# Optimization experiments

Measured on AMD Instinct MI355X. Metric: run time of the kernel, lower is better.

## Reference

```python
import jax, jax.numpy as jnp
import numpy as np

CONSTRAINT_WEIGHT = 0.5
FOCAL_GAMMA = 2.0
EPS = 1e-8

B, G, C = 65536, 9, 9
BLK = 3  # int(sqrt(G))


def setup_inputs() -> dict:
    key = jax.random.key(0)
    k1, k2, k3 = jax.random.split(key, 3)
    logits = jax.random.normal(k1, (B, G, G, C), dtype=jnp.float32)
    targets = jax.random.randint(k2, (B, G, G), 0, 10, dtype=jnp.int64)
    puzzles = jax.random.randint(k3, (B, G, G), 0, 10, dtype=jnp.int64)
    return {"logits": logits, "targets": targets, "puzzles": puzzles}


def _sudoku_loss(logits, targets, puzzles):
    b, g, _, c = logits.shape
    mask = (puzzles == 0).astype(logits.dtype)            # [B,G,G]
    tgt = jnp.clip(targets - 1, 0, c - 1)                 # [B,G,G]

    log_probs = jax.nn.log_softmax(logits, axis=-1)       # [B,G,G,C]
    probs = jnp.exp(log_probs)

    # --- focal CE over masked (empty) cells ---
    lp_t = jnp.take_along_axis(log_probs, tgt[..., None], axis=-1)[..., 0]  # [B,G,G]
    pt = jnp.exp(lp_t)
    ce = -lp_t
    focal = (1.0 - pt) ** FOCAL_GAMMA * ce
    msum = mask.sum()
    ce_loss = (focal * mask).sum() / (msum + EPS)

    # --- constraint loss ---
    masked_probs = probs * mask[..., None]                # [B,G,G,C]
    row_sums = masked_probs.sum(axis=2)                   # [B,G,C]
    row_loss = jnp.mean((row_sums - 1.0) ** 2)
    col_sums = masked_probs.sum(axis=1)                   # [B,G,C]
    col_loss = jnp.mean((col_sums - 1.0) ** 2)
    # boxes: [B, br, r, bc, c_in, C] -> sum over the 3x3 cells of each box
    box = masked_probs.reshape(b, BLK, BLK, BLK, BLK, c)
    box_sums = box.transpose(0, 1, 3, 2, 4, 5).reshape(b, BLK * BLK, BLK * BLK, c).sum(axis=2)
    box_loss = jnp.mean((box_sums - 1.0) ** 2)

    entropy = -(probs * log_probs).sum(axis=-1)           # [B,G,G]
    entropy_loss = 0.1 * ((entropy * mask).sum() / (msum + EPS))

    top2, _ = jax.lax.top_k(probs, 2)                     # [B,G,G,2]
    gap = top2[..., 0] - top2[..., 1]
    uniqueness_loss = 0.1 * jnp.mean(jax.nn.relu(1.0 - gap))

    constraint_loss = (row_loss + col_loss + box_loss + entropy_loss + uniqueness_loss) * 0.2
    return ce_loss + CONSTRAINT_WEIGHT * constraint_loss


def reference(logits, targets, puzzles):
    return _sudoku_loss(logits, targets, puzzles)
```

## Files before the change

### kernel.cpp

```cpp
#include <hip/hip_runtime.h>

#define THREADS 256
#define PB 3
#define NPAIR 5
#define COLW 84
#define MAXGRID 2048

typedef float f4 __attribute__((ext_vector_type(4)));
typedef f4 f4a4 __attribute__((aligned(4)));
typedef __fp16 h2 __attribute__((ext_vector_type(2)));
typedef unsigned int u32;
typedef u32 u32x4 __attribute__((ext_vector_type(4)));

static __device__ __forceinline__ u32 pkrtz(float a, float b) {
  h2 v = __builtin_amdgcn_cvt_pkrtz(a, b);
  return __builtin_bit_cast(u32, v);
}

__global__ __launch_bounds__(THREADS) void sudoku_main(
    const float* __restrict__ logits,
    const int*   __restrict__ targets,
    const int*   __restrict__ puzzles,
    float* __restrict__ partial,
    int B)
{
  __shared__ u32 probT[2][PB * NPAIR * COLW];
  __shared__ float sred[4][5];

  const int tid  = threadIdx.x;
  const int lp   = tid / 81;
  const int cell = tid % 81;
  const bool workerA = tid < 243;
  const int cpad = 28 * (cell / 27) + (cell % 27);
  const int B81  = B * 81;
  const int numGroups = (B + PB - 1) / PB;

  const int lane = tid & 63;
  const int wv   = tid >> 6;
  const int clp  = lane / NPAIR;
  const int cpr  = lane % NPAIR;

  float a_focal = 0.f, a_ent = 0.f, a_msk = 0.f, a_uniq = 0.f, a_sq = 0.f;

  bool vA = workerA && (blockIdx.x * 243 + tid < B81);
  f4 c0{}, c1{}; float c8 = 0.f; int ctg = 0, cpz = 0;
  if (vA) {
    const float* Lp = logits + (size_t)(blockIdx.x * 243 + tid) * 9;
    c0 = *(const f4a4*)Lp; c1 = *(const f4a4*)(Lp + 4); c8 = Lp[8];
    ctg = targets[blockIdx.x * 243 + tid]; cpz = puzzles[blockIdx.x * 243 + tid];
  }

  int it = 0;
  for (int g = blockIdx.x; g < numGroups; g += gridDim.x, ++it) {
    u32* PT = probT[it & 1];

    if (vA) {
      float l[9];
      l[0]=c0[0]; l[1]=c0[1]; l[2]=c0[2]; l[3]=c0[3];
      l[4]=c1[0]; l[5]=c1[1]; l[6]=c1[2]; l[7]=c1[3]; l[8]=c8;
      int tg = ctg - 1; tg = tg < 0 ? 0 : (tg > 8 ? 8 : tg);

      float t1 = l[0], t2 = -3.0e38f;
#pragma unroll
      for (int i = 1; i < 9; ++i) {
        float hi = fmaxf(t1, l[i]);
        float lo = fminf(t1, l[i]);
        t1 = hi; t2 = fmaxf(t2, lo);
      }
      float e[9], s = 0.f, lsum = 0.f, ltg = l[0];
#pragma unroll
      for (int i = 0; i < 9; ++i) {
        float x  = l[i] - t1;
        float ei = __expf(x);
        e[i] = ei; s += ei;
        lsum = fmaf(ei, x, lsum);
        if (i > 0) ltg = (tg == i) ? l[i] : ltg;
      }
      float inv_s = __builtin_amdgcn_rcpf(s);
      float logs  = __logf(s);
      float lpt   = (ltg - t1) - logs;
      float pt    = __expf(lpt);
      float om    = 1.f - pt;
      float focal = om * om * (-lpt);
      float ent   = logs - lsum * inv_s;
      float gap   = (1.f - __expf(t2 - t1)) * inv_s;
      float uq    = fmaxf(0.f, 1.f - gap);
      float mk    = (cpz == 0) ? 1.f : 0.f;
      a_focal += focal * mk;
      a_ent   += ent * mk;
      a_msk   += mk;
      a_uniq  += uq;
      float pm = inv_s * mk;

      const int wbase = lp * (NPAIR * COLW) + cpad;
      PT[wbase + 0*COLW] = pkrtz(e[0]*pm, e[1]*pm);
      PT[wbase + 1*COLW] = pkrtz(e[2]*pm, e[3]*pm);
      PT[wbase + 2*COLW] = pkrtz(e[4]*pm, e[5]*pm);
      PT[wbase + 3*COLW] = pkrtz(e[6]*pm, e[7]*pm);
      PT[wbase + 4*COLW] = pkrtz(e[8]*pm, 0.f);
    }

    const int gn = g + (int)gridDim.x;
    const bool vAn = workerA && (gn < numGroups) && (gn * 243 + tid < B81);
    f4 n0{}, n1{}; float n8 = 0.f; int ntg = 0, npz = 0;
    if (vAn) {
      const float* Lp = logits + (size_t)(gn * 243 + tid) * 9;
      n0 = *(const f4a4*)Lp; n1 = *(const f4a4*)(Lp + 4); n8 = Lp[8];
      ntg = targets[gn * 243 + tid]; npz = puzzles[gn * 243 + tid];
    }

    __syncthreads();

    if (wv == (it & 3) && lane < PB * NPAIR && (g * PB + clp) < B) {
      const u32* base = PT + (clp * NPAIR + cpr) * COLW;
      h2 hz; hz[0] = (__fp16)0.f; hz[1] = (__fp16)0.f;
      h2 rs[9], cs[9], bs[9];
#pragma unroll
      for (int u = 0; u < 9; ++u) { rs[u] = hz; cs[u] = hz; bs[u] = hz; }
#pragma unroll
      for (int b = 0; b < 3; ++b) {
        u32x4 w[7];
#pragma unroll
        for (int q = 0; q < 7; ++q) w[q] = *(const u32x4*)(base + b * 28 + q * 4);
#pragma unroll
        for (int j = 0; j < 27; ++j) {
          h2 v = __builtin_bit_cast(h2, w[j >> 2][j & 3]);
          rs[3 * b + j / 9]       += v;
          cs[j % 9]               += v;
          bs[3 * b + (j % 9) / 3] += v;
        }
      }
      const float hiw = (cpr == NPAIR - 1) ? 0.f : 1.f;
      float sq = 0.f;
#pragma unroll
      for (int u = 0; u < 9; ++u) {
        float x;
        x = (float)rs[u][0] - 1.f; sq = fmaf(x, x, sq);
        x = (float)cs[u][0] - 1.f; sq = fmaf(x, x, sq);
        x = (float)bs[u][0] - 1.f; sq = fmaf(x, x, sq);
        x = (float)rs[u][1] - 1.f; sq = fmaf(hiw * x, x, sq);
        x = (float)cs[u][1] - 1.f; sq = fmaf(hiw * x, x, sq);
        x = (float)bs[u][1] - 1.f; sq = fmaf(hiw * x, x, sq);
      }
      a_sq += sq;
    }

    vA = vAn; c0 = n0; c1 = n1; c8 = n8; ctg = ntg; cpz = npz;
  }

#pragma unroll
  for (int off = 32; off > 0; off >>= 1) {
    a_focal += __shfl_down(a_focal, off);
    a_ent   += __shfl_down(a_ent,   off);
    a_msk   += __shfl_down(a_msk,   off);
    a_uniq  += __shfl_down(a_uniq,  off);
    a_sq    += __shfl_down(a_sq,    off);
  }
  if (lane == 0) {
    sred[wv][0] = a_focal; sred[wv][1] = a_ent; sred[wv][2] = a_msk;
    sred[wv][3] = a_uniq;  sred[wv][4] = a_sq;
  }
  __syncthreads();
  if (tid < 5) {
    float v = sred[0][tid] + sred[1][tid] + sred[2][tid] + sred[3][tid];
    partial[(size_t)blockIdx.x * 8 + tid] = v;
  }
}

__global__ __launch_bounds__(256) void sudoku_finalize(
    const float* __restrict__ partial, float* __restrict__ out,
    int nblk, float invBG)
{
  __shared__ float sb[4][5];
  const int tid = threadIdx.x;
  float s[5] = {0.f, 0.f, 0.f, 0.f, 0.f};
  for (int b = tid; b < nblk; b += 256) {
    const float* row = partial + (size_t)b * 8;
#pragma unroll
    for (int u = 0; u < 5; ++u) s[u] += row[u];
  }
#pragma unroll
  for (int off = 32; off > 0; off >>= 1)
#pragma unroll
    for (int u = 0; u < 5; ++u) s[u] += __shfl_down(s[u], off);
  const int wv = tid >> 6, lane = tid & 63;
  if (lane == 0) {
#pragma unroll
    for (int u = 0; u < 5; ++u) sb[wv][u] = s[u];
  }
  __syncthreads();
  if (tid == 0) {
    float focal = sb[0][0] + sb[1][0] + sb[2][0] + sb[3][0];
    float ent   = sb[0][1] + sb[1][1] + sb[2][1] + sb[3][1];
    float msum  = sb[0][2] + sb[1][2] + sb[2][2] + sb[3][2];
    float uniq  = sb[0][3] + sb[1][3] + sb[2][3] + sb[3][3];
    float sq    = sb[0][4] + sb[1][4] + sb[2][4] + sb[3][4];
    float inv_m = 1.f / (msum + 1e-8f);
    float ce    = focal * inv_m;
    float entl  = 0.1f * ent * inv_m;
    float uql   = 0.1f * uniq * invBG;
    float rcb   = sq * invBG;
    float constraint = (rcb + entl + uql) * 0.2f;
    out[0] = ce + 0.5f * constraint;
  }
}

extern "C" void kernel_launch(void* const* d_in, const int* in_sizes, int n_in,
                              void* d_out, int out_size, void* d_ws, size_t ws_size,
                              hipStream_t stream)
{
  (void)n_in; (void)out_size; (void)ws_size;
  const float* logits  = (const float*)d_in[0];
  const int*   targets = (const int*)d_in[1];
  const int*   puzzles = (const int*)d_in[2];
  float* out = (float*)d_out;
  float* partial = (float*)d_ws;

  const int B = in_sizes[0] / 729;
  const int numGroups = (B + PB - 1) / PB;
  int grid = numGroups < MAXGRID ? numGroups : MAXGRID;

  sudoku_main<<<grid, THREADS, 0, stream>>>(logits, targets, puzzles, partial, B);

  const float invBG = 1.f / ((float)B * 81.f);
  sudoku_finalize<<<1, 256, 0, stream>>>(partial, out, grid, invBG);
}
```

Baseline: 58.30 us.

## Stage logits through LDS with coalesced float4 loads, one 12-puzzle tile per block

Drops the persistent grid-stride loop with register prefetch. Each block now copies a contiguous 12-puzzle chunk of logits into shared memory using fully coalesced float4 loads, and each thread then processes 4 consecutive cells read from LDS. Targets and puzzles are read as int4 vectors. Packed fp16 probabilities overwrite the same LDS buffer, and the finalize kernel uses a column-major partial layout with 1024 threads. This trades the cross-iteration load/compute overlap for coalesced vector loads, more blocks, and larger LDS use per block, which may reduce occupancy and cause bank conflicts on the stride-9 reads.

```diff
diff --git a/kernel.cpp b/kernel.cpp
--- a/kernel.cpp
+++ b/kernel.cpp
@@ -1,16 +1,15 @@
 #include <hip/hip_runtime.h>
 
 #define THREADS 256
-#define PB 3
-#define NPAIR 5
-#define COLW 84
-#define MAXGRID 2048
+#define PB 12
+#define CELLS_PB (PB * 81)
+#define WORKERS 243
+#define TOTW (CELLS_PB * 9)
 
 typedef float f4 __attribute__((ext_vector_type(4)));
-typedef f4 f4a4 __attribute__((aligned(4)));
 typedef __fp16 h2 __attribute__((ext_vector_type(2)));
 typedef unsigned int u32;
-typedef u32 u32x4 __attribute__((ext_vector_type(4)));
+typedef int i4 __attribute__((ext_vector_type(4)));
 
 static __device__ __forceinline__ u32 pkrtz(float a, float b) {
   h2 v = __builtin_amdgcn_cvt_pkrtz(a, b);
@@ -22,43 +21,48 @@
     const int*   __restrict__ targets,
     const int*   __restrict__ puzzles,
     float* __restrict__ partial,
-    int B)
+    int B, int ngrid)
 {
-  __shared__ u32 probT[2][PB * NPAIR * COLW];
+  __shared__ float buf[TOTW];
   __shared__ float sred[4][5];
 
-  const int tid  = threadIdx.x;
-  const int lp   = tid / 81;
-  const int cell = tid % 81;
-  const bool workerA = tid < 243;
-  const int cpad = 28 * (cell / 27) + (cell % 27);
-  const int B81  = B * 81;
-  const int numGroups = (B + PB - 1) / PB;
-
-  const int lane = tid & 63;
-  const int wv   = tid >> 6;
-  const int clp  = lane / NPAIR;
-  const int cpr  = lane % NPAIR;
-
-  float a_focal = 0.f, a_ent = 0.f, a_msk = 0.f, a_uniq = 0.f, a_sq = 0.f;
-
-  bool vA = workerA && (blockIdx.x * 243 + tid < B81);
-  f4 c0{}, c1{}; float c8 = 0.f; int ctg = 0, cpz = 0;
+  const int tid = threadIdx.x;
+  const int g   = blockIdx.x;
+  const long totalCells = (long)B * 81;
+
+  float a_focal=0.f, a_ent=0.f, a_msk=0.f, a_uniq=0.f, a_sq=0.f;
+
+  if (tid < WORKERS) {
+    const size_t gbase4 = (size_t)g * (TOTW / 4);
+    const size_t lim4   = (size_t)(totalCells * 9 / 4);
+    const f4* src = (const f4*)logits;
+#pragma unroll
+    for (int r = 0; r < 9; ++r) {
+      size_t idx = gbase4 + r * WORKERS + tid;
+      if (idx < lim4) ((f4*)buf)[r * WORKERS + tid] = src[idx];
+    }
+  }
+
+  const long cell0 = (long)g * CELLS_PB + 4 * tid;
+  const bool vA = (tid < WORKERS) && (cell0 < totalCells);
+  i4 tg4{}, pz4{};
   if (vA) {
-    const float* Lp = logits + (size_t)(blockIdx.x * 243 + tid) * 9;
-    c0 = *(const f4a4*)Lp; c1 = *(const f4a4*)(Lp + 4); c8 = Lp[8];
-    ctg = targets[blockIdx.x * 243 + tid]; cpz = puzzles[blockIdx.x * 243 + tid];
-  }
-
-  int it = 0;
-  for (int g = blockIdx.x; g < numGroups; g += gridDim.x, ++it) {
-    u32* PT = probT[it & 1];
-
-    if (vA) {
+    tg4 = *(const i4*)(targets + cell0);
+    pz4 = *(const i4*)(puzzles + cell0);
+  }
+  __syncthreads();
+
+  if (vA) {
+    f4 s[9];
+#pragma unroll
+    for (int q = 0; q < 9; ++q) s[q] = ((const f4*)buf)[tid * 9 + q];
+
+#pragma unroll
+    for (int k = 0; k < 4; ++k) {
       float l[9];
-      l[0]=c0[0]; l[1]=c0[1]; l[2]=c0[2]; l[3]=c0[3];
-      l[4]=c1[0]; l[5]=c1[1]; l[6]=c1[2]; l[7]=c1[3]; l[8]=c8;
-      int tg = ctg - 1; tg = tg < 0 ? 0 : (tg > 8 ? 8 : tg);
+#pragma unroll
+      for (int i = 0; i < 9; ++i) { const int w = 9 * k + i; l[i] = s[w >> 2][w & 3]; }
+      int tg = tg4[k] - 1; tg = tg < 0 ? 0 : (tg > 8 ? 8 : tg);
 
       float t1 = l[0], t2 = -3.0e38f;
 #pragma unroll
@@ -67,17 +71,17 @@
         float lo = fminf(t1, l[i]);
         t1 = hi; t2 = fmaxf(t2, lo);
       }
-      float e[9], s = 0.f, lsum = 0.f, ltg = l[0];
+      float e[9], ssum = 0.f, lsum = 0.f, ltg = l[0];
 #pragma unroll
       for (int i = 0; i < 9; ++i) {
         float x  = l[i] - t1;
         float ei = __expf(x);
-        e[i] = ei; s += ei;
+        e[i] = ei; ssum += ei;
         lsum = fmaf(ei, x, lsum);
         if (i > 0) ltg = (tg == i) ? l[i] : ltg;
       }
-      float inv_s = __builtin_amdgcn_rcpf(s);
-      float logs  = __logf(s);
+      float inv_s = __builtin_amdgcn_rcpf(ssum);
+      float logs  = __logf(ssum);
       float lpt   = (ltg - t1) - logs;
       float pt    = __expf(lpt);
       float om    = 1.f - pt;
@@ -85,52 +89,40 @@
       float ent   = logs - lsum * inv_s;
       float gap   = (1.f - __expf(t2 - t1)) * inv_s;
       float uq    = fmaxf(0.f, 1.f - gap);
-      float mk    = (cpz == 0) ? 1.f : 0.f;
+      float mk    = (pz4[k] == 0) ? 1.f : 0.f;
       a_focal += focal * mk;
       a_ent   += ent * mk;
       a_msk   += mk;
       a_uniq  += uq;
       float pm = inv_s * mk;
 
-      const int wbase = lp * (NPAIR * COLW) + cpad;
-      PT[wbase + 0*COLW] = pkrtz(e[0]*pm, e[1]*pm);
-      PT[wbase + 1*COLW] = pkrtz(e[2]*pm, e[3]*pm);
-      PT[wbase + 2*COLW] = pkrtz(e[4]*pm, e[5]*pm);
-      PT[wbase + 3*COLW] = pkrtz(e[6]*pm, e[7]*pm);
-      PT[wbase + 4*COLW] = pkrtz(e[8]*pm, 0.f);
-    }
-
-    const int gn = g + (int)gridDim.x;
-    const bool vAn = workerA && (gn < numGroups) && (gn * 243 + tid < B81);
-    f4 n0{}, n1{}; float n8 = 0.f; int ntg = 0, npz = 0;
-    if (vAn) {
-      const float* Lp = logits + (size_t)(gn * 243 + tid) * 9;
-      n0 = *(const f4a4*)Lp; n1 = *(const f4a4*)(Lp + 4); n8 = Lp[8];
-      ntg = targets[gn * 243 + tid]; npz = puzzles[gn * 243 + tid];
-    }
-
-    __syncthreads();
-
-    if (wv == (it & 3) && lane < PB * NPAIR && (g * PB + clp) < B) {
-      const u32* base = PT + (clp * NPAIR + cpr) * COLW;
+      u32* pw = (u32*)buf + (size_t)(4 * tid + k) * 9;
+      pw[0] = pkrtz(e[0] * pm, e[1] * pm);
+      pw[1] = pkrtz(e[2] * pm, e[3] * pm);
+      pw[2] = pkrtz(e[4] * pm, e[5] * pm);
+      pw[3] = pkrtz(e[6] * pm, e[7] * pm);
+      pw[4] = pkrtz(e[8] * pm, 0.f);
+    }
+  }
+  __syncthreads();
+
+  if (tid < PB * 5) {
+    const int pz = tid / 5, pr = tid - 5 * pz;
+    if ((long)g * PB + pz < B) {
+      const u32* cb = (const u32*)buf;
       h2 hz; hz[0] = (__fp16)0.f; hz[1] = (__fp16)0.f;
       h2 rs[9], cs[9], bs[9];
 #pragma unroll
       for (int u = 0; u < 9; ++u) { rs[u] = hz; cs[u] = hz; bs[u] = hz; }
-#pragma unroll
-      for (int b = 0; b < 3; ++b) {
-        u32x4 w[7];
-#pragma unroll
-        for (int q = 0; q < 7; ++q) w[q] = *(const u32x4*)(base + b * 28 + q * 4);
-#pragma unroll
-        for (int j = 0; j < 27; ++j) {
-          h2 v = __builtin_bit_cast(h2, w[j >> 2][j & 3]);
-          rs[3 * b + j / 9]       += v;
-          cs[j % 9]               += v;
-          bs[3 * b + (j % 9) / 3] += v;
-        }
-      }
-      const float hiw = (cpr == NPAIR - 1) ? 0.f : 1.f;
+      const int base = pz * 729 + pr;
+#pragma unroll
+      for (int j = 0; j < 81; ++j) {
+        h2 v = __builtin_bit_cast(h2, cb[base + 9 * j]);
+        rs[j / 9]                    += v;
+        cs[j % 9]                    += v;
+        bs[(j / 27) * 3 + (j % 9) / 3] += v;
+      }
+      const float hiw = (pr == 4) ? 0.f : 1.f;
       float sq = 0.f;
 #pragma unroll
       for (int u = 0; u < 9; ++u) {
@@ -144,8 +136,6 @@
       }
       a_sq += sq;
     }
-
-    vA = vAn; c0 = n0; c1 = n1; c8 = n8; ctg = ntg; cpz = npz;
   }
 
 #pragma unroll
@@ -156,6 +146,7 @@
     a_uniq  += __shfl_down(a_uniq,  off);
     a_sq    += __shfl_down(a_sq,    off);
   }
+  const int wv = tid >> 6, lane = tid & 63;
   if (lane == 0) {
     sred[wv][0] = a_focal; sred[wv][1] = a_ent; sred[wv][2] = a_msk;
     sred[wv][3] = a_uniq;  sred[wv][4] = a_sq;
@@ -163,21 +154,20 @@
   __syncthreads();
   if (tid < 5) {
     float v = sred[0][tid] + sred[1][tid] + sred[2][tid] + sred[3][tid];
-    partial[(size_t)blockIdx.x * 8 + tid] = v;
-  }
-}
-
-__global__ __launch_bounds__(256) void sudoku_finalize(
+    partial[(size_t)tid * ngrid + g] = v;
+  }
+}
+
+__global__ __launch_bounds__(1024) void sudoku_finalize(
     const float* __restrict__ partial, float* __restrict__ out,
-    int nblk, float invBG)
+    int ngrid, float invBG)
 {
-  __shared__ float sb[4][5];
+  __shared__ float sb[16][5];
   const int tid = threadIdx.x;
   float s[5] = {0.f, 0.f, 0.f, 0.f, 0.f};
-  for (int b = tid; b < nblk; b += 256) {
-    const float* row = partial + (size_t)b * 8;
-#pragma unroll
-    for (int u = 0; u < 5; ++u) s[u] += row[u];
+  for (int b = tid; b < ngrid; b += 1024) {
+#pragma unroll
+    for (int u = 0; u < 5; ++u) s[u] += partial[(size_t)u * ngrid + b];
   }
 #pragma unroll
   for (int off = 32; off > 0; off >>= 1)
@@ -190,11 +180,12 @@
   }
   __syncthreads();
   if (tid == 0) {
-    float focal = sb[0][0] + sb[1][0] + sb[2][0] + sb[3][0];
-    float ent   = sb[0][1] + sb[1][1] + sb[2][1] + sb[3][1];
-    float msum  = sb[0][2] + sb[1][2] + sb[2][2] + sb[3][2];
-    float uniq  = sb[0][3] + sb[1][3] + sb[2][3] + sb[3][3];
-    float sq    = sb[0][4] + sb[1][4] + sb[2][4] + sb[3][4];
+    float focal = 0.f, ent = 0.f, msum = 0.f, uniq = 0.f, sq = 0.f;
+#pragma unroll
+    for (int w = 0; w < 16; ++w) {
+      focal += sb[w][0]; ent += sb[w][1]; msum += sb[w][2];
+      uniq  += sb[w][3]; sq  += sb[w][4];
+    }
     float inv_m = 1.f / (msum + 1e-8f);
     float ce    = focal * inv_m;
     float entl  = 0.1f * ent * inv_m;
@@ -217,11 +208,11 @@
   float* partial = (float*)d_ws;
 
   const int B = in_sizes[0] / 729;
-  const int numGroups = (B + PB - 1) / PB;
-  int grid = numGroups < MAXGRID ? numGroups : MAXGRID;
-
-  sudoku_main<<<grid, THREADS, 0, stream>>>(logits, targets, puzzles, partial, B);
+  const long totalCells = (long)B * 81;
+  const int ngrid = (int)((totalCells + CELLS_PB - 1) / CELLS_PB);
+
+  sudoku_main<<<ngrid, THREADS, 0, stream>>>(logits, targets, puzzles, partial, B, ngrid);
 
   const float invBG = 1.f / ((float)B * 81.f);
-  sudoku_finalize<<<1, 256, 0, stream>>>(partial, out, grid, invBG);
-}
+  sudoku_finalize<<<1, 1024, 0, stream>>>(partial, out, ngrid, invBG);
+}
```

New measurement: 57.20 us. No clear change (-1.9%).
